# Optimization experiments

Hardware: AMD Instinct MI355X
Metric: run time of the kernel (lower is better)

The kernel has to match this reference:

```python
import jax, jax.numpy as jnp
import numpy as np

B, S, E, A = 8, 127, 512, 256  # batch, seq (pre-sentinel), encoder dim, arc representation dim

_BRANCHES = ["sib_head", "sib_dep", "cop_head", "cop_dep", "gp_head", "gp_dep", "gp_head_dep"]


def setup_inputs() -> dict:
    key = jax.random.key(0)
    ks = jax.random.split(key, 16)
    d = {
        "x": jax.random.normal(ks[0], (B, S, E), jnp.float32),
        "pos_tags": jax.random.randint(ks[1], (B, S), 0, 48),
        "mask": jnp.ones((B, S), jnp.int32),
    }
    for i, n in enumerate(_BRANCHES):
        d[f"W_{n}"] = jax.random.normal(ks[2 + i], (E, A), jnp.float32) * (1.0 / np.sqrt(E))
        d[f"b_{n}"] = jnp.zeros((A,), jnp.float32)
    for i, n in enumerate(["sib", "cop", "gp"]):
        d[f"U_{n}"] = jax.random.normal(ks[9 + i], (A, A, A), jnp.float32) * (1.0 / A)
    d["sentinel"] = jax.random.normal(ks[12], (E,), jnp.float32)
    return d


def _tri(u, v, w, U):
    # trilinear (triaffine) score: s[b,i,j,k] = sum_{a,c,d} u[b,i,a] U[a,c,d] v[b,j,c] w[b,k,d]
    t = jnp.einsum('bia,acd->bicd', u, U)       # [B, n, A, A]
    t = jnp.einsum('bicd,bjc->bijd', t, v)      # [B, n, n, A]
    return jnp.einsum('bijd,bkd->bijk', t, w)   # [B, n, n, n]


def reference(x, pos_tags, mask,
              W_sib_head, b_sib_head, W_sib_dep, b_sib_dep,
              W_cop_head, b_cop_head, W_cop_dep, b_cop_dep,
              W_gp_head, b_gp_head, W_gp_dep, b_gp_dep,
              W_gp_head_dep, b_gp_head_dep,
              U_sib, U_cop, U_gp, sentinel):
    b, _, e = x.shape
    # prepend head sentinel token
    h = jnp.concatenate([jnp.broadcast_to(sentinel, (b, 1, e)), x], axis=1)  # [B, n, E]
    mask_full = jnp.concatenate([jnp.ones((b, 1), mask.dtype), mask], axis=1)
    elu = jax.nn.elu
    sib_head = elu(h @ W_sib_head + b_sib_head)
    sib_dep = elu(h @ W_sib_dep + b_sib_dep)
    cop_head = elu(h @ W_cop_head + b_cop_head)
    cop_dep = elu(h @ W_cop_dep + b_cop_dep)
    gp_head = elu(h @ W_gp_head + b_gp_head)
    gp_dep = elu(h @ W_gp_dep + b_gp_dep)
    gp_head_dep = elu(h @ W_gp_head_dep + b_gp_head_dep)
    sib = _tri(sib_head, sib_dep, sib_dep, U_sib)
    cop = _tri(cop_head, cop_dep, cop_head, U_cop)
    gp = _tri(gp_head, gp_head_dep, gp_dep, U_gp)
    return sib, cop, gp, mask_full
```

## Files before the change

### kernel.cpp

```cpp
#include <hip/hip_runtime.h>
#include <math.h>

#define N_TOK 128
#define ADIM  256
#define EDIM  512
#define BSZ   8
#define NSQ   65536

typedef short bf16x8 __attribute__((ext_vector_type(8)));
typedef float f32x4  __attribute__((ext_vector_type(4)));
#define MFMA_BF16(a, b, c) __builtin_amdgcn_mfma_f32_16x16x32_bf16((a), (b), (c), 0, 0, 0)

__device__ inline short f2bf(float f) {
  union { float f; unsigned u; } v; v.f = f;
  unsigned r = v.u + 0x7fff + ((v.u >> 16) & 1);
  return (short)(r >> 16);
}

typedef const __attribute__((address_space(1))) unsigned int* gas_ptr;
typedef __attribute__((address_space(3))) unsigned int* las_ptr;
__device__ __forceinline__ void gload16(const void* g, void* l) {
  __builtin_amdgcn_global_load_lds((gas_ptr)g, (las_ptr)l, 16, 0, 0);
}

struct ProjArgs {
  const float* W[7];
  const float* b[7];
};

__global__ __launch_bounds__(256) void proj_kernel(
    const float* __restrict__ x, const float* __restrict__ sentinel,
    ProjArgs args, short* __restrict__ proj)
{
  const int p  = blockIdx.y;
  const int m0 = blockIdx.x * 8;
  const int tid = threadIdx.x;
  __shared__ float hs[8][EDIM];
  #pragma unroll
  for (int q = 0; q < 16; ++q) {
    int idx = tid + q * 256;
    int r = idx >> 9, c = idx & 511;
    int m = m0 + r, b = m >> 7, i = m & 127;
    hs[r][c] = (i == 0) ? sentinel[c] : x[((size_t)(b * 127) + (i - 1)) * EDIM + c];
  }
  __syncthreads();
  const float* W = args.W[p];
  float bias = args.b[p][tid];
  float acc[8];
  #pragma unroll
  for (int r = 0; r < 8; ++r) acc[r] = bias;
  #pragma unroll 4
  for (int k = 0; k < EDIM; ++k) {
    float wv = W[(size_t)k * ADIM + tid];
    #pragma unroll
    for (int r = 0; r < 8; ++r) acc[r] = fmaf(hs[r][k], wv, acc[r]);
  }
  short* outp = proj + ((size_t)p * (BSZ * N_TOK) + m0) * ADIM + tid;
  #pragma unroll
  for (int r = 0; r < 8; ++r) {
    float v = acc[r];
    v = v > 0.f ? v : expm1f(v);
    outp[(size_t)r * ADIM] = f2bf(v);
  }
}

__global__ __launch_bounds__(256) void permU(
    const float* __restrict__ U, short* __restrict__ Ut)
{
  __shared__ float tile[64][69];
  const int c  = blockIdx.x;
  const int a0 = blockIdx.y * 64;
  const int d0 = blockIdx.z * 64;
  const int t  = threadIdx.x;
  {
    int ar = t >> 4, ds4 = (t & 15) * 4;
    #pragma unroll
    for (int q = 0; q < 4; ++q) {
      int a = ar + q * 16;
      float4 v = *(const float4*)&U[(size_t)(a0 + a) * NSQ + c * 256 + d0 + ds4];
      tile[a][ds4] = v.x; tile[a][ds4 + 1] = v.y;
      tile[a][ds4 + 2] = v.z; tile[a][ds4 + 3] = v.w;
    }
  }
  __syncthreads();
  {
    int dr = t >> 4, as4 = (t & 15) * 4;
    #pragma unroll
    for (int q = 0; q < 4; ++q) {
      int d = dr + q * 16;
      ushort4 o;
      o.x = (unsigned short)f2bf(tile[as4 + 0][d]);
      o.y = (unsigned short)f2bf(tile[as4 + 1][d]);
      o.z = (unsigned short)f2bf(tile[as4 + 2][d]);
      o.w = (unsigned short)f2bf(tile[as4 + 3][d]);
      *(ushort4*)&Ut[((size_t)(d0 + d) * 256 + c) * 256 + a0 + as4] = o;
    }
  }
}


__global__ __launch_bounds__(256) void gemm_t1(
    const short* __restrict__ A,
    const short* __restrict__ Ut,
    short* __restrict__ C)
{
  __shared__ short As[128 * 32];
  __shared__ short Bs[128 * 32];
  const int tid = threadIdx.x;
  const int wave = tid >> 6, lane = tid & 63;
  const int ln15 = lane & 15, quad = lane >> 4;
  const int m0 = blockIdx.x * 128, n0 = blockIdx.y * 128;
  const int wm = (wave & 1) * 64, wn = (wave >> 1) * 64;
  const int q0 = tid,        r0 = q0 >> 2, s0 = (q0 & 3) ^ ((r0 >> 1) & 3);
  const int q1 = tid + 256,  r1 = q1 >> 2, s1 = (q1 & 3) ^ ((r1 >> 1) & 3);
  const int rdoff = ((quad ^ ((ln15 >> 1) & 3)) << 3);
  f32x4 acc[4][4] = {};
  for (int kt = 0; kt < ADIM; kt += 32) {
    __syncthreads();
    gload16(&A [(size_t)(m0 + r0) * ADIM + kt + s0 * 8], &As[q0 * 8]);
    gload16(&A [(size_t)(m0 + r1) * ADIM + kt + s1 * 8], &As[q1 * 8]);
    gload16(&Ut[(size_t)(n0 + r0) * ADIM + kt + s0 * 8], &Bs[q0 * 8]);
    gload16(&Ut[(size_t)(n0 + r1) * ADIM + kt + s1 * 8], &Bs[q1 * 8]);
    __syncthreads();
    bf16x8 af[4], bfr[4];
    #pragma unroll
    for (int r = 0; r < 4; ++r)  af[r]  = *(bf16x8*)&As[(wm + r * 16 + ln15) * 32 + rdoff];
    #pragma unroll
    for (int c2 = 0; c2 < 4; ++c2) bfr[c2] = *(bf16x8*)&Bs[(wn + c2 * 16 + ln15) * 32 + rdoff];
    #pragma unroll
    for (int r = 0; r < 4; ++r)
      #pragma unroll
      for (int c2 = 0; c2 < 4; ++c2)
        acc[r][c2] = MFMA_BF16(bfr[c2], af[r], acc[r][c2]);
  }
  #pragma unroll
  for (int r = 0; r < 4; ++r)
    #pragma unroll
    for (int c2 = 0; c2 < 4; ++c2) {
      int m = m0 + wm + r * 16 + ln15;
      int n = n0 + wn + c2 * 16 + quad * 4;
      ushort4 o;
      o.x = (unsigned short)f2bf(acc[r][c2][0]);
      o.y = (unsigned short)f2bf(acc[r][c2][1]);
      o.z = (unsigned short)f2bf(acc[r][c2][2]);
      o.w = (unsigned short)f2bf(acc[r][c2][3]);
      *(ushort4*)&C[(size_t)m * NSQ + n] = o;
    }
}

__global__ __launch_bounds__(256) void gemm_t2(
    const short* __restrict__ t1,
    const short* __restrict__ projv,
    short* __restrict__ t2)
{
  __shared__ short As[128 * 32];
  __shared__ short Bs[128 * 32];
  const int tid = threadIdx.x;
  const int wave = tid >> 6, lane = tid & 63;
  const int ln15 = lane & 15, quad = lane >> 4;
  const int n0 = blockIdx.x * 128;
  const int bl = blockIdx.y;
  const short* Bt = t1 + (size_t)bl * N_TOK * NSQ;
  const short* Av = projv + (size_t)bl * N_TOK * ADIM;
  const int wm = (wave & 1) * 64, wn = (wave >> 1) * 64;
  const int q0 = tid,        r0 = q0 >> 2, s0 = (q0 & 3) ^ ((r0 >> 1) & 3);
  const int q1 = tid + 256,  r1 = q1 >> 2, s1 = (q1 & 3) ^ ((r1 >> 1) & 3);
  const int rdoff = ((quad ^ ((ln15 >> 1) & 3)) << 3);
  f32x4 acc[4][4] = {};
  for (int kt = 0; kt < ADIM; kt += 32) {
    __syncthreads();
    gload16(&Av[(size_t)r0 * ADIM + kt + s0 * 8],        &As[q0 * 8]);
    gload16(&Av[(size_t)r1 * ADIM + kt + s1 * 8],        &As[q1 * 8]);
    gload16(&Bt[(size_t)(n0 + r0) * ADIM + kt + s0 * 8], &Bs[q0 * 8]);
    gload16(&Bt[(size_t)(n0 + r1) * ADIM + kt + s1 * 8], &Bs[q1 * 8]);
    __syncthreads();
    bf16x8 af[4], bfr[4];
    #pragma unroll
    for (int r = 0; r < 4; ++r)  af[r]  = *(bf16x8*)&As[(wm + r * 16 + ln15) * 32 + rdoff];
    #pragma unroll
    for (int c2 = 0; c2 < 4; ++c2) bfr[c2] = *(bf16x8*)&Bs[(wn + c2 * 16 + ln15) * 32 + rdoff];
    #pragma unroll
    for (int r = 0; r < 4; ++r)
      #pragma unroll
      for (int c2 = 0; c2 < 4; ++c2)
        acc[r][c2] = MFMA_BF16(bfr[c2], af[r], acc[r][c2]);
  }
  const int i     = n0 >> 8;
  const int dbase = n0 & 255;
  short* ob = t2 + (size_t)bl * (N_TOK * N_TOK * ADIM) + (size_t)i * (N_TOK * ADIM);
  #pragma unroll
  for (int r = 0; r < 4; ++r)
    #pragma unroll
    for (int c2 = 0; c2 < 4; ++c2) {
      int j = wm + r * 16 + ln15;
      int d = dbase + wn + c2 * 16 + quad * 4;
      ushort4 o;
      o.x = (unsigned short)f2bf(acc[r][c2][0]);
      o.y = (unsigned short)f2bf(acc[r][c2][1]);
      o.z = (unsigned short)f2bf(acc[r][c2][2]);
      o.w = (unsigned short)f2bf(acc[r][c2][3]);
      *(ushort4*)&ob[(size_t)j * ADIM + d] = o;
    }
}

__global__ __launch_bounds__(256) void gemm_s(
    const short* __restrict__ t2,
    const short* __restrict__ projw,
    float* __restrict__ out)
{
  __shared__ short As[128 * 32];
  __shared__ short Bs[128 * 32];
  const int tid = threadIdx.x;
  const int wave = tid >> 6, lane = tid & 63;
  const int ln15 = lane & 15, quad = lane >> 4;
  const int m0 = blockIdx.x * 128;
  const int bl = blockIdx.y;
  const short* At = t2 + (size_t)bl * (N_TOK * N_TOK * ADIM);
  const short* Bw = projw + (size_t)bl * N_TOK * ADIM;
  float* ob = out + (size_t)bl * N_TOK * N_TOK * N_TOK + (size_t)m0 * N_TOK;
  const int wm = (wave & 1) * 64, wn = (wave >> 1) * 64;
  const int q0 = tid,        r0 = q0 >> 2, s0 = (q0 & 3) ^ ((r0 >> 1) & 3);
  const int q1 = tid + 256,  r1 = q1 >> 2, s1 = (q1 & 3) ^ ((r1 >> 1) & 3);
  const int rdoff = ((quad ^ ((ln15 >> 1) & 3)) << 3);
  f32x4 acc[4][4] = {};
  for (int kt = 0; kt < ADIM; kt += 32) {
    __syncthreads();
    gload16(&At[(size_t)(m0 + r0) * ADIM + kt + s0 * 8], &As[q0 * 8]);
    gload16(&At[(size_t)(m0 + r1) * ADIM + kt + s1 * 8], &As[q1 * 8]);
    gload16(&Bw[(size_t)r0 * ADIM + kt + s0 * 8],        &Bs[q0 * 8]);
    gload16(&Bw[(size_t)r1 * ADIM + kt + s1 * 8],        &Bs[q1 * 8]);
    __syncthreads();
    bf16x8 af[4], bfr[4];
    #pragma unroll
    for (int r = 0; r < 4; ++r)  af[r]  = *(bf16x8*)&As[(wm + r * 16 + ln15) * 32 + rdoff];
    #pragma unroll
    for (int c2 = 0; c2 < 4; ++c2) bfr[c2] = *(bf16x8*)&Bs[(wn + c2 * 16 + ln15) * 32 + rdoff];
    #pragma unroll
    for (int r = 0; r < 4; ++r)
      #pragma unroll
      for (int c2 = 0; c2 < 4; ++c2)
        acc[r][c2] = MFMA_BF16(bfr[c2], af[r], acc[r][c2]);
  }
  #pragma unroll
  for (int r = 0; r < 4; ++r)
    #pragma unroll
    for (int c2 = 0; c2 < 4; ++c2) {
      int m = wm + r * 16 + ln15;
      int k = wn + c2 * 16 + quad * 4;
      *(f32x4*)&ob[(size_t)m * N_TOK + k] = acc[r][c2];
    }
}

__global__ void mask_kernel(const int* __restrict__ mask, float* __restrict__ out) {
  int idx = blockIdx.x * 256 + threadIdx.x;
  if (idx < BSZ * N_TOK) {
    int b = idx >> 7, i = idx & 127;
    out[idx] = (i == 0) ? 1.0f : (float)mask[b * 127 + i - 1];
  }
}

extern "C" void kernel_launch(void* const* d_in, const int* in_sizes, int n_in,
                              void* d_out, int out_size, void* d_ws, size_t ws_size,
                              hipStream_t stream)
{
  const float* x    = (const float*)d_in[0];
  const int*   mask = (const int*)d_in[2];
  ProjArgs pa;
  for (int p = 0; p < 7; ++p) {
    pa.W[p] = (const float*)d_in[3 + 2 * p];
    pa.b[p] = (const float*)d_in[4 + 2 * p];
  }
  const float* Us[3] = {(const float*)d_in[17], (const float*)d_in[18],
                        (const float*)d_in[19]};
  const float* sentinel = (const float*)d_in[20];

  short* proj = (short*)d_ws;
  const size_t ut_off = 4u << 20;
  const size_t t1_off = ut_off + ((size_t)NSQ * ADIM * 2);
  const size_t t2_off = t1_off + ((size_t)1024 * NSQ * 2);
  short* Ut = (short*)((char*)d_ws + ut_off);
  short* t1 = (short*)((char*)d_ws + t1_off);
  short* t2 = (short*)((char*)d_ws + t2_off);

  proj_kernel<<<dim3(128, 7), 256, 0, stream>>>(x, sentinel, pa, proj);

  const int u_idx[3] = {0, 2, 4};
  const int v_idx[3] = {1, 3, 6};
  const int w_idx[3] = {1, 2, 5};
  float* outp = (float*)d_out;

  for (int sc = 0; sc < 3; ++sc) {
    permU<<<dim3(256, 4, 4), 256, 0, stream>>>(Us[sc], Ut);
    gemm_t1<<<dim3(8, 512), 256, 0, stream>>>(
        proj + (size_t)u_idx[sc] * 1024 * ADIM, Ut, t1);
    gemm_t2<<<dim3(256, 8), 256, 0, stream>>>(
        t1, proj + (size_t)v_idx[sc] * 1024 * ADIM, t2);
    gemm_s<<<dim3(128, 8), 256, 0, stream>>>(
        t2, proj + (size_t)w_idx[sc] * 1024 * ADIM,
        outp + (size_t)sc * BSZ * N_TOK * N_TOK * N_TOK);
  }
  mask_kernel<<<dim3(4), 256, 0, stream>>>(
      mask, outp + (size_t)3 * BSZ * N_TOK * N_TOK * N_TOK);
}
```

Baseline: 885.7 us.

## Fuse second and third trilinear GEMMs through LDS, batch U permutes, remap t1 grid

```diff
diff --git a/kernel.cpp b/kernel.cpp
--- a/kernel.cpp
+++ b/kernel.cpp
@@ -27,6 +27,9 @@
   const float* W[7];
   const float* b[7];
 };
+struct UArgs {
+  const float* U[3];
+};
 
 __global__ __launch_bounds__(256) void proj_kernel(
     const float* __restrict__ x, const float* __restrict__ sentinel,
@@ -64,13 +67,17 @@
   }
 }
 
-__global__ __launch_bounds__(256) void permU(
-    const float* __restrict__ U, short* __restrict__ Ut)
+__global__ __launch_bounds__(256) void permU_all(
+    UArgs ua, short* __restrict__ UtAll)
 {
   __shared__ float tile[64][69];
   const int c  = blockIdx.x;
   const int a0 = blockIdx.y * 64;
-  const int d0 = blockIdx.z * 64;
+  const int z  = blockIdx.z;
+  const int sc = z >> 2;
+  const int d0 = (z & 3) * 64;
+  const float* U = ua.U[sc];
+  short* Ut = UtAll + (size_t)sc * NSQ * ADIM;
   const int t  = threadIdx.x;
   {
     int ar = t >> 4, ds4 = (t & 15) * 4;
@@ -98,7 +105,6 @@
   }
 }
 
-
 __global__ __launch_bounds__(256) void gemm_t1(
     const short* __restrict__ A,
     const short* __restrict__ Ut,
@@ -109,7 +115,9 @@
   const int tid = threadIdx.x;
   const int wave = tid >> 6, lane = tid & 63;
   const int ln15 = lane & 15, quad = lane >> 4;
-  const int m0 = blockIdx.x * 128, n0 = blockIdx.y * 128;
+  const int h = blockIdx.x;
+  const int l = (h & 7) * 512 + (h >> 3);
+  const int m0 = (l & 7) * 128, n0 = (l >> 3) * 128;
   const int wm = (wave & 1) * 64, wn = (wave >> 1) * 64;
   const int q0 = tid,        r0 = q0 >> 2, s0 = (q0 & 3) ^ ((r0 >> 1) & 3);
   const int q1 = tid + 256,  r1 = q1 >> 2, s1 = (q1 & 3) ^ ((r1 >> 1) & 3);
@@ -148,106 +156,97 @@
     }
 }
 
-__global__ __launch_bounds__(256) void gemm_t2(
+__global__ __launch_bounds__(256) void fuse_ts(
     const short* __restrict__ t1,
     const short* __restrict__ projv,
-    short* __restrict__ t2)
+    const short* __restrict__ projw,
+    float* __restrict__ out)
 {
   __shared__ short As[128 * 32];
   __shared__ short Bs[128 * 32];
+  __shared__ short t2s[128 * 256];
   const int tid = threadIdx.x;
   const int wave = tid >> 6, lane = tid & 63;
   const int ln15 = lane & 15, quad = lane >> 4;
-  const int n0 = blockIdx.x * 128;
+  const int i  = blockIdx.x;
   const int bl = blockIdx.y;
-  const short* Bt = t1 + (size_t)bl * N_TOK * NSQ;
+  const short* Bt = t1 + (size_t)(bl * N_TOK + i) * NSQ;
   const short* Av = projv + (size_t)bl * N_TOK * ADIM;
+  const short* Bw = projw + (size_t)bl * N_TOK * ADIM;
+  float* ob = out + (size_t)(bl * N_TOK + i) * N_TOK * N_TOK;
   const int wm = (wave & 1) * 64, wn = (wave >> 1) * 64;
   const int q0 = tid,        r0 = q0 >> 2, s0 = (q0 & 3) ^ ((r0 >> 1) & 3);
   const int q1 = tid + 256,  r1 = q1 >> 2, s1 = (q1 & 3) ^ ((r1 >> 1) & 3);
   const int rdoff = ((quad ^ ((ln15 >> 1) & 3)) << 3);
-  f32x4 acc[4][4] = {};
-  for (int kt = 0; kt < ADIM; kt += 32) {
+
+  for (int dh = 0; dh < 2; ++dh) {
+    f32x4 acc[4][4] = {};
+    for (int ct = 0; ct < ADIM; ct += 32) {
+      __syncthreads();
+      gload16(&Av[(size_t)r0 * ADIM + ct + s0 * 8],              &As[q0 * 8]);
+      gload16(&Av[(size_t)r1 * ADIM + ct + s1 * 8],              &As[q1 * 8]);
+      gload16(&Bt[(size_t)(dh * 128 + r0) * ADIM + ct + s0 * 8], &Bs[q0 * 8]);
+      gload16(&Bt[(size_t)(dh * 128 + r1) * ADIM + ct + s1 * 8], &Bs[q1 * 8]);
+      __syncthreads();
+      bf16x8 af[4], bfr[4];
+      #pragma unroll
+      for (int r = 0; r < 4; ++r)
+        af[r]  = *(bf16x8*)&As[(wm + r * 16 + ln15) * 32 + rdoff];
+      #pragma unroll
+      for (int c2 = 0; c2 < 4; ++c2)
+        bfr[c2] = *(bf16x8*)&Bs[(wn + c2 * 16 + ln15) * 32 + rdoff];
+      #pragma unroll
+      for (int r = 0; r < 4; ++r)
+        #pragma unroll
+        for (int c2 = 0; c2 < 4; ++c2)
+          acc[r][c2] = MFMA_BF16(bfr[c2], af[r], acc[r][c2]);
+    }
+    #pragma unroll
+    for (int r = 0; r < 4; ++r)
+      #pragma unroll
+      for (int c2 = 0; c2 < 4; ++c2) {
+        int j  = wm + r * 16 + ln15;
+        int d  = dh * 128 + wn + c2 * 16 + quad * 4;
+        int sp = (d >> 3) ^ (j & 7);
+        ushort4 o;
+        o.x = (unsigned short)f2bf(acc[r][c2][0]);
+        o.y = (unsigned short)f2bf(acc[r][c2][1]);
+        o.z = (unsigned short)f2bf(acc[r][c2][2]);
+        o.w = (unsigned short)f2bf(acc[r][c2][3]);
+        *(ushort4*)((char*)t2s + (size_t)j * 512 + sp * 16 + (quad & 1) * 8) = o;
+      }
+  }
+  __syncthreads();
+
+  f32x4 acc2[4][4] = {};
+  for (int dt = 0; dt < ADIM; dt += 32) {
+    if (dt) __syncthreads();
+    gload16(&Bw[(size_t)r0 * ADIM + dt + s0 * 8], &Bs[q0 * 8]);
+    gload16(&Bw[(size_t)r1 * ADIM + dt + s1 * 8], &Bs[q1 * 8]);
     __syncthreads();
-    gload16(&Av[(size_t)r0 * ADIM + kt + s0 * 8],        &As[q0 * 8]);
-    gload16(&Av[(size_t)r1 * ADIM + kt + s1 * 8],        &As[q1 * 8]);
-    gload16(&Bt[(size_t)(n0 + r0) * ADIM + kt + s0 * 8], &Bs[q0 * 8]);
-    gload16(&Bt[(size_t)(n0 + r1) * ADIM + kt + s1 * 8], &Bs[q1 * 8]);
-    __syncthreads();
-    bf16x8 af[4], bfr[4];
-    #pragma unroll
-    for (int r = 0; r < 4; ++r)  af[r]  = *(bf16x8*)&As[(wm + r * 16 + ln15) * 32 + rdoff];
-    #pragma unroll
-    for (int c2 = 0; c2 < 4; ++c2) bfr[c2] = *(bf16x8*)&Bs[(wn + c2 * 16 + ln15) * 32 + rdoff];
-    #pragma unroll
-    for (int r = 0; r < 4; ++r)
-      #pragma unroll
-      for (int c2 = 0; c2 < 4; ++c2)
-        acc[r][c2] = MFMA_BF16(bfr[c2], af[r], acc[r][c2]);
-  }
-  const int i     = n0 >> 8;
-  const int dbase = n0 & 255;
-  short* ob = t2 + (size_t)bl * (N_TOK * N_TOK * ADIM) + (size_t)i * (N_TOK * ADIM);
-  #pragma unroll
-  for (int r = 0; r < 4; ++r)
-    #pragma unroll
-    for (int c2 = 0; c2 < 4; ++c2) {
-      int j = wm + r * 16 + ln15;
-      int d = dbase + wn + c2 * 16 + quad * 4;
-      ushort4 o;
-      o.x = (unsigned short)f2bf(acc[r][c2][0]);
-      o.y = (unsigned short)f2bf(acc[r][c2][1]);
-      o.z = (unsigned short)f2bf(acc[r][c2][2]);
-      o.w = (unsigned short)f2bf(acc[r][c2][3]);
-      *(ushort4*)&ob[(size_t)j * ADIM + d] = o;
-    }
-}
-
-__global__ __launch_bounds__(256) void gemm_s(
-    const short* __restrict__ t2,
-    const short* __restrict__ projw,
-    float* __restrict__ out)
-{
-  __shared__ short As[128 * 32];
-  __shared__ short Bs[128 * 32];
-  const int tid = threadIdx.x;
-  const int wave = tid >> 6, lane = tid & 63;
-  const int ln15 = lane & 15, quad = lane >> 4;
-  const int m0 = blockIdx.x * 128;
-  const int bl = blockIdx.y;
-  const short* At = t2 + (size_t)bl * (N_TOK * N_TOK * ADIM);
-  const short* Bw = projw + (size_t)bl * N_TOK * ADIM;
-  float* ob = out + (size_t)bl * N_TOK * N_TOK * N_TOK + (size_t)m0 * N_TOK;
-  const int wm = (wave & 1) * 64, wn = (wave >> 1) * 64;
-  const int q0 = tid,        r0 = q0 >> 2, s0 = (q0 & 3) ^ ((r0 >> 1) & 3);
-  const int q1 = tid + 256,  r1 = q1 >> 2, s1 = (q1 & 3) ^ ((r1 >> 1) & 3);
-  const int rdoff = ((quad ^ ((ln15 >> 1) & 3)) << 3);
-  f32x4 acc[4][4] = {};
-  for (int kt = 0; kt < ADIM; kt += 32) {
-    __syncthreads();
-    gload16(&At[(size_t)(m0 + r0) * ADIM + kt + s0 * 8], &As[q0 * 8]);
-    gload16(&At[(size_t)(m0 + r1) * ADIM + kt + s1 * 8], &As[q1 * 8]);
-    gload16(&Bw[(size_t)r0 * ADIM + kt + s0 * 8],        &Bs[q0 * 8]);
-    gload16(&Bw[(size_t)r1 * ADIM + kt + s1 * 8],        &Bs[q1 * 8]);
-    __syncthreads();
-    bf16x8 af[4], bfr[4];
-    #pragma unroll
-    for (int r = 0; r < 4; ++r)  af[r]  = *(bf16x8*)&As[(wm + r * 16 + ln15) * 32 + rdoff];
-    #pragma unroll
-    for (int c2 = 0; c2 < 4; ++c2) bfr[c2] = *(bf16x8*)&Bs[(wn + c2 * 16 + ln15) * 32 + rdoff];
-    #pragma unroll
-    for (int r = 0; r < 4; ++r)
-      #pragma unroll
-      for (int c2 = 0; c2 < 4; ++c2)
-        acc[r][c2] = MFMA_BF16(bfr[c2], af[r], acc[r][c2]);
-  }
-  #pragma unroll
-  for (int r = 0; r < 4; ++r)
-    #pragma unroll
-    for (int c2 = 0; c2 < 4; ++c2) {
-      int m = wm + r * 16 + ln15;
-      int k = wn + c2 * 16 + quad * 4;
-      *(f32x4*)&ob[(size_t)m * N_TOK + k] = acc[r][c2];
+    bf16x8 a2[4], b2[4];
+    #pragma unroll
+    for (int fr = 0; fr < 4; ++fr) {
+      int j  = wm + fr * 16 + ln15;
+      int sp = ((dt >> 3) + quad) ^ (j & 7);
+      a2[fr] = *(bf16x8*)((char*)t2s + (size_t)j * 512 + sp * 16);
+    }
+    #pragma unroll
+    for (int fc = 0; fc < 4; ++fc)
+      b2[fc] = *(bf16x8*)&Bs[(wn + fc * 16 + ln15) * 32 + rdoff];
+    #pragma unroll
+    for (int fr = 0; fr < 4; ++fr)
+      #pragma unroll
+      for (int fc = 0; fc < 4; ++fc)
+        acc2[fr][fc] = MFMA_BF16(b2[fc], a2[fr], acc2[fr][fc]);
+  }
+  #pragma unroll
+  for (int fr = 0; fr < 4; ++fr)
+    #pragma unroll
+    for (int fc = 0; fc < 4; ++fc) {
+      int j = wm + fr * 16 + ln15;
+      int k = wn + fc * 16 + quad * 4;
+      *(f32x4*)&ob[(size_t)j * N_TOK + k] = acc2[fr][fc];
     }
 }
 
@@ -270,19 +269,20 @@
     pa.W[p] = (const float*)d_in[3 + 2 * p];
     pa.b[p] = (const float*)d_in[4 + 2 * p];
   }
-  const float* Us[3] = {(const float*)d_in[17], (const float*)d_in[18],
-                        (const float*)d_in[19]};
+  UArgs ua;
+  ua.U[0] = (const float*)d_in[17];
+  ua.U[1] = (const float*)d_in[18];
+  ua.U[2] = (const float*)d_in[19];
   const float* sentinel = (const float*)d_in[20];
 
   short* proj = (short*)d_ws;
   const size_t ut_off = 4u << 20;
-  const size_t t1_off = ut_off + ((size_t)NSQ * ADIM * 2);
-  const size_t t2_off = t1_off + ((size_t)1024 * NSQ * 2);
-  short* Ut = (short*)((char*)d_ws + ut_off);
-  short* t1 = (short*)((char*)d_ws + t1_off);
-  short* t2 = (short*)((char*)d_ws + t2_off);
+  const size_t t1_off = ut_off + 3 * ((size_t)NSQ * ADIM * 2);
+  short* UtAll = (short*)((char*)d_ws + ut_off);
+  short* t1    = (short*)((char*)d_ws + t1_off);
 
   proj_kernel<<<dim3(128, 7), 256, 0, stream>>>(x, sentinel, pa, proj);
+  permU_all<<<dim3(256, 4, 12), 256, 0, stream>>>(ua, UtAll);
 
   const int u_idx[3] = {0, 2, 4};
   const int v_idx[3] = {1, 3, 6};
@@ -290,13 +290,13 @@
   float* outp = (float*)d_out;
 
   for (int sc = 0; sc < 3; ++sc) {
-    permU<<<dim3(256, 4, 4), 256, 0, stream>>>(Us[sc], Ut);
-    gemm_t1<<<dim3(8, 512), 256, 0, stream>>>(
-        proj + (size_t)u_idx[sc] * 1024 * ADIM, Ut, t1);
-    gemm_t2<<<dim3(256, 8), 256, 0, stream>>>(
-        t1, proj + (size_t)v_idx[sc] * 1024 * ADIM, t2);
-    gemm_s<<<dim3(128, 8), 256, 0, stream>>>(
-        t2, proj + (size_t)w_idx[sc] * 1024 * ADIM,
+    gemm_t1<<<dim3(4096), 256, 0, stream>>>(
+        proj + (size_t)u_idx[sc] * 1024 * ADIM,
+        UtAll + (size_t)sc * NSQ * ADIM, t1);
+    fuse_ts<<<dim3(128, 8), 256, 0, stream>>>(
+        t1,
+        proj + (size_t)v_idx[sc] * 1024 * ADIM,
+        proj + (size_t)w_idx[sc] * 1024 * ADIM,
         outp + (size_t)sc * BSZ * N_TOK * N_TOK * N_TOK);
   }
   mask_kernel<<<dim3(4), 256, 0, stream>>>(
```

Result: no change. 869.8 us (-1.8%).
